# Kernel optimization log

Measured on AMD Instinct MI355X. Metric: run time of the kernel, lower is better.

## Reference

```python
import jax, jax.numpy as jnp
import numpy as np

N, E, G = 100000, 1600000, 64   # nodes, edges, graphs
IN, H, OUT = 32, 128, 3


def setup_inputs() -> dict:
    key = jax.random.key(0)
    ks = jax.random.split(key, 24)
    def w(k, i, o):
        return (jax.random.normal(k, (i, o), jnp.float32) / np.sqrt(i)).astype(jnp.float32)
    inp = {
        "x": jax.random.normal(ks[0], (N, IN), jnp.float32),
        "edge_index": jax.random.randint(ks[1], (2, E), 0, N, dtype=jnp.int32).astype(jnp.int64),
        "batch": jnp.sort(jax.random.randint(ks[2], (N,), 0, G, dtype=jnp.int32)).astype(jnp.int64),
        # SAGEConv layer 0 (in->hidden): lin_l (neighbors, with bias), lin_r (root, no bias)
        "Wl0": w(ks[3], IN, H), "bl0": jnp.zeros((H,), jnp.float32), "Wr0": w(ks[4], IN, H),
        # SAGEConv layers 1,2 (hidden->hidden)
        "Wl1": w(ks[5], H, H), "bl1": jnp.zeros((H,), jnp.float32), "Wr1": w(ks[6], H, H),
        "Wl2": w(ks[7], H, H), "bl2": jnp.zeros((H,), jnp.float32), "Wr2": w(ks[8], H, H),
        # output head
        "Wfc": w(ks[9], H, OUT), "bfc": jnp.zeros((OUT,), jnp.float32),
        # aux MLP on (dim1, dim3)
        "Wa1": w(ks[10], 2, H), "ba1": jnp.zeros((H,), jnp.float32),
        "Wa2": w(ks[11], H, H), "ba2": jnp.zeros((H,), jnp.float32),
        "Wao": w(ks[12], H, 1), "bao": jnp.zeros((1,), jnp.float32),
    }
    return inp


def _sage_conv(x, src, dst, Wl, bl, Wr):
    # PyG SAGEConv (mean aggr): out = lin_l(mean_{j in N(i)} x_j) + lin_r(x_i)
    msg = x[src]                                   # [E, d] gather
    agg = jax.ops.segment_sum(msg, dst, num_segments=N)
    cnt = jax.ops.segment_sum(jnp.ones((src.shape[0],), x.dtype), dst, num_segments=N)
    mean = agg / jnp.maximum(cnt, 1.0)[:, None]
    return mean @ Wl + bl + x @ Wr


def reference(x, edge_index, batch,
              Wl0, bl0, Wr0, Wl1, bl1, Wr1, Wl2, bl2, Wr2,
              Wfc, bfc, Wa1, ba1, Wa2, ba2, Wao, bao):
    src, dst = edge_index[0], edge_index[1]
    h = jax.nn.relu(_sage_conv(x, src, dst, Wl0, bl0, Wr0))   # dropout is identity in eval
    h = jax.nn.relu(_sage_conv(h, src, dst, Wl1, bl1, Wr1))
    h = jax.nn.relu(_sage_conv(h, src, dst, Wl2, bl2, Wr2))
    main = h @ Wfc + bfc                                      # [N, 3]
    dim1, dim3 = main[:, 0], main[:, 2]
    aux_in = jnp.stack([dim1, dim3], axis=-1)                 # [N, 2]
    a = jax.nn.relu(aux_in @ Wa1 + ba1)
    a = jax.nn.relu(a @ Wa2 + ba2)
    aux_out = (a @ Wao + bao)[:, 0]                           # [N]
    final = jnp.stack([dim1, aux_out, dim3], axis=-1)         # [N, 3]
    # global mean pool over graph ids
    s = jax.ops.segment_sum(final, batch, num_segments=G)
    c = jax.ops.segment_sum(jnp.ones((final.shape[0],), final.dtype), batch, num_segments=G)
    return s / jnp.maximum(c, 1.0)[:, None]                   # [G, 3]
```

## Files before the change

kernel.cpp:

```cpp
#include <hip/hip_runtime.h>

#define NR 128
#define PART_CH 4096
typedef unsigned short ushortT;
typedef __attribute__((ext_vector_type(8))) short short8;
typedef __attribute__((ext_vector_type(4))) float float4v;
typedef __attribute__((ext_vector_type(2))) float float2v;

__device__ __forceinline__ unsigned short f32_to_bf16_rne(float f) {
    unsigned u = __float_as_uint(f);
    unsigned r = (u + 0x7fffu + ((u >> 16) & 1u)) >> 16;
    return (unsigned short)r;
}

__device__ __forceinline__ unsigned char f32_to_fp8(float f) {
    return (unsigned char)(__builtin_amdgcn_cvt_pk_fp8_f32(f, f, 0, false) & 0xff);
}

__device__ __forceinline__ void accum8(float* acc, uint4 v) {
    unsigned u[4] = {v.x, v.y, v.z, v.w};
#pragma unroll
    for (int q = 0; q < 4; q++) {
        acc[2 * q]     += __uint_as_float(u[q] << 16);
        acc[2 * q + 1] += __uint_as_float(u[q] & 0xffff0000u);
    }
}

__device__ __forceinline__ void accum16_fp8(float* acc, uint4 v) {
    unsigned u[4] = {v.x, v.y, v.z, v.w};
#pragma unroll
    for (int q = 0; q < 4; q++) {
        float2v lo = __builtin_amdgcn_cvt_pk_f32_fp8(u[q], false);
        float2v hi = __builtin_amdgcn_cvt_pk_f32_fp8(u[q], true);
        acc[4 * q + 0] += lo.x;
        acc[4 * q + 1] += lo.y;
        acc[4 * q + 2] += hi.x;
        acc[4 * q + 3] += hi.y;
    }
}


__launch_bounds__(256)
__global__ void bucket_count(const int* __restrict__ dst, int* __restrict__ bcnt, int E, int NB) {
    __shared__ int h[1024];
    int t = threadIdx.x;
    for (int j = t; j < NB; j += 256) h[j] = 0;
    __syncthreads();
    int e0 = blockIdx.x * PART_CH;
    int e1 = min(e0 + PART_CH, E);
    for (int e = e0 + t; e < e1; e += 256) atomicAdd(&h[dst[e] >> 7], 1);
    __syncthreads();
    for (int j = t; j < NB; j += 256) {
        int v = h[j];
        if (v) atomicAdd(&bcnt[j], v);
    }
}

__launch_bounds__(256)
__global__ void bucket_scan(const int* __restrict__ bcnt, int* __restrict__ bstart,
                            int* __restrict__ gcur, int NB, int E) {
    __shared__ int sh[256];
    int t = threadIdx.x;
    int v[4];
    int tot = 0;
#pragma unroll
    for (int j = 0; j < 4; j++) {
        int idx = t * 4 + j;
        v[j] = (idx < NB) ? bcnt[idx] : 0;
        tot += v[j];
    }
    sh[t] = tot;
    __syncthreads();
    for (int off = 1; off < 256; off <<= 1) {
        int add = (t >= off) ? sh[t - off] : 0;
        __syncthreads();
        sh[t] += add;
        __syncthreads();
    }
    int run = sh[t] - tot;
#pragma unroll
    for (int j = 0; j < 4; j++) {
        int idx = t * 4 + j;
        if (idx < NB) { bstart[idx] = run; gcur[idx] = run; }
        run += v[j];
    }
    if (t == 0) bstart[NB] = E;
}

__launch_bounds__(256)
__global__ void partition_edges(const int* __restrict__ src, const int* __restrict__ dst,
                                int* __restrict__ gcur, unsigned* __restrict__ packed,
                                int E, int NB) {
    __shared__ int hist[1024];
    __shared__ int base[1024];
    int t = threadIdx.x;
    int e0 = blockIdx.x * PART_CH;
    int e1 = min(e0 + PART_CH, E);
    for (int j = t; j < NB; j += 256) hist[j] = 0;
    __syncthreads();
    for (int e = e0 + t; e < e1; e += 256) atomicAdd(&hist[dst[e] >> 7], 1);
    __syncthreads();
    for (int j = t; j < NB; j += 256) {
        int h = hist[j];
        base[j] = h ? atomicAdd(&gcur[j], h) : 0;
    }
    __syncthreads();
    for (int j = t; j < NB; j += 256) hist[j] = base[j];
    __syncthreads();
    for (int e = e0 + t; e < e1; e += 256) {
        int d = dst[e];
        int b = d >> 7;
        int pos = atomicAdd(&hist[b], 1);
        packed[pos] = (unsigned)src[e] | ((unsigned)(d & (NR - 1)) << 17);
    }
}

__launch_bounds__(256)
__global__ void bucket_sort(const unsigned* __restrict__ packed, const int* __restrict__ bstart,
                            int* __restrict__ row_start, int* __restrict__ srcs, int N) {
    __shared__ int cnt[NR];
    __shared__ int sc[NR];
    __shared__ int cur[NR];
    int b = blockIdx.x, t = threadIdx.x;
    int nb0 = b * NR;
    int nnode = min(NR, N - nb0);
    int lo = bstart[b], hi = bstart[b + 1];
    if (t < NR) cnt[t] = 0;
    __syncthreads();
    for (int j = lo + t; j < hi; j += 256) atomicAdd(&cnt[packed[j] >> 17], 1);
    __syncthreads();
    if (t < NR) sc[t] = cnt[t];
    __syncthreads();
    for (int off = 1; off < NR; off <<= 1) {
        int add = (t >= off && t < NR) ? sc[t - off] : 0;
        __syncthreads();
        if (t < NR) sc[t] += add;
        __syncthreads();
    }
    if (t < nnode) {
        int s = lo + sc[t] - cnt[t];
        row_start[nb0 + t] = s;
        cur[t] = s;
    }
    if (t == 0 && nb0 + nnode == N) row_start[N] = hi;
    __syncthreads();
    for (int j = lo + t; j < hi; j += 256) {
        unsigned pk = packed[j];
        int pos = atomicAdd(&cur[pk >> 17], 1);
        srcs[pos] = (int)(pk & 0x1FFFFu);
    }
}


__global__ void to_bf16_vec(const float* __restrict__ in, ushortT* __restrict__ out, int n4) {
    int t = blockIdx.x * 256 + threadIdx.x;
    if (t < n4) {
        float4 v = ((const float4*)in)[t];
        ushort4 o;
        o.x = f32_to_bf16_rne(v.x);
        o.y = f32_to_bf16_rne(v.y);
        o.z = f32_to_bf16_rne(v.z);
        o.w = f32_to_bf16_rne(v.w);
        ((ushort4*)out)[t] = o;
    }
}


__global__ void prep_wt(const float* __restrict__ Wl, const float* __restrict__ Wr,
                        ushortT* __restrict__ Wt, int KH) {
    int KT = 2 * KH;
    int tid = blockIdx.x * 256 + threadIdx.x;
    if (tid >= 128 * KT) return;
    int col = tid / KT, k = tid - col * KT;
    float v = (k < KH) ? Wl[k * 128 + col] : Wr[(k - KH) * 128 + col];
    int pos = (k + 8 * col) & (KT - 1);
    Wt[col * KT + pos] = f32_to_bf16_rne(v);
}

__global__ void prep_w1(const float* __restrict__ W, ushortT* __restrict__ Wt) {
    int tid = blockIdx.x * 256 + threadIdx.x;
    if (tid >= 128 * 128) return;
    int col = tid >> 7, k = tid & 127;
    int pos = (k + 8 * col) & 127;
    Wt[col * 128 + pos] = f32_to_bf16_rne(W[k * 128 + col]);
}


template <int CPN>
__launch_bounds__(256)
__global__ void aggregate_mean_bf16(const uint4* __restrict__ hin, ushortT* __restrict__ out,
                                    const int* __restrict__ srcs, const int* __restrict__ rs, int n) {
    constexpr int TPN = CPN / 2;
    int tid = blockIdx.x * 256 + threadIdx.x;
    if (tid >= n * TPN) return;
    int i = tid / TPN;
    int c = tid & (TPN - 1);
    int lo = rs[i], hi = rs[i + 1];
    float acc0[8], acc1[8];
#pragma unroll
    for (int q = 0; q < 8; q++) { acc0[q] = 0.f; acc1[q] = 0.f; }
    int e = lo;
    for (; e + 8 <= hi; e += 8) {
        int s[8];
#pragma unroll
        for (int u = 0; u < 8; u++) s[u] = srcs[e + u];
        uint4 va[8], vb[8];
#pragma unroll
        for (int u = 0; u < 8; u++) {
            va[u] = hin[(size_t)s[u] * CPN + c];
            vb[u] = hin[(size_t)s[u] * CPN + c + TPN];
        }
#pragma unroll
        for (int u = 0; u < 8; u++) { accum8(acc0, va[u]); accum8(acc1, vb[u]); }
    }
    for (; e + 4 <= hi; e += 4) {
        int s[4];
#pragma unroll
        for (int u = 0; u < 4; u++) s[u] = srcs[e + u];
        uint4 va[4], vb[4];
#pragma unroll
        for (int u = 0; u < 4; u++) {
            va[u] = hin[(size_t)s[u] * CPN + c];
            vb[u] = hin[(size_t)s[u] * CPN + c + TPN];
        }
#pragma unroll
        for (int u = 0; u < 4; u++) { accum8(acc0, va[u]); accum8(acc1, vb[u]); }
    }
    for (; e < hi; ++e) {
        int s = srcs[e];
        accum8(acc0, hin[(size_t)s * CPN + c]);
        accum8(acc1, hin[(size_t)s * CPN + c + TPN]);
    }
    float inv = 1.0f / (float)max(hi - lo, 1);
    uint4 o0, o1;
    o0.x = (unsigned)f32_to_bf16_rne(acc0[0] * inv) | ((unsigned)f32_to_bf16_rne(acc0[1] * inv) << 16);
    o0.y = (unsigned)f32_to_bf16_rne(acc0[2] * inv) | ((unsigned)f32_to_bf16_rne(acc0[3] * inv) << 16);
    o0.z = (unsigned)f32_to_bf16_rne(acc0[4] * inv) | ((unsigned)f32_to_bf16_rne(acc0[5] * inv) << 16);
    o0.w = (unsigned)f32_to_bf16_rne(acc0[6] * inv) | ((unsigned)f32_to_bf16_rne(acc0[7] * inv) << 16);
    o1.x = (unsigned)f32_to_bf16_rne(acc1[0] * inv) | ((unsigned)f32_to_bf16_rne(acc1[1] * inv) << 16);
    o1.y = (unsigned)f32_to_bf16_rne(acc1[2] * inv) | ((unsigned)f32_to_bf16_rne(acc1[3] * inv) << 16);
    o1.z = (unsigned)f32_to_bf16_rne(acc1[4] * inv) | ((unsigned)f32_to_bf16_rne(acc1[5] * inv) << 16);
    o1.w = (unsigned)f32_to_bf16_rne(acc1[6] * inv) | ((unsigned)f32_to_bf16_rne(acc1[7] * inv) << 16);
    ((uint4*)out)[(size_t)i * CPN + c] = o0;
    ((uint4*)out)[(size_t)i * CPN + c + TPN] = o1;
}


__launch_bounds__(256)
__global__ void aggregate_mean_fp8(const uint4* __restrict__ hin, ushortT* __restrict__ out,
                                   const int* __restrict__ srcs, const int* __restrict__ rs, int n) {
    int tid = blockIdx.x * 256 + threadIdx.x;
    if (tid >= n * 8) return;
    int i = tid >> 3;
    int c = tid & 7;
    int lo = rs[i], hi = rs[i + 1];
    float acc[16];
#pragma unroll
    for (int q = 0; q < 16; q++) acc[q] = 0.f;
    int e = lo;
    for (; e + 8 <= hi; e += 8) {
        int s[8];
#pragma unroll
        for (int u = 0; u < 8; u++) s[u] = srcs[e + u];
        uint4 v[8];
#pragma unroll
        for (int u = 0; u < 8; u++) v[u] = hin[(size_t)s[u] * 8 + c];
#pragma unroll
        for (int u = 0; u < 8; u++) accum16_fp8(acc, v[u]);
    }
    for (; e + 4 <= hi; e += 4) {
        int s[4];
#pragma unroll
        for (int u = 0; u < 4; u++) s[u] = srcs[e + u];
        uint4 v[4];
#pragma unroll
        for (int u = 0; u < 4; u++) v[u] = hin[(size_t)s[u] * 8 + c];
#pragma unroll
        for (int u = 0; u < 4; u++) accum16_fp8(acc, v[u]);
    }
    for (; e < hi; ++e) accum16_fp8(acc, hin[(size_t)srcs[e] * 8 + c]);
    float inv = 1.0f / (float)max(hi - lo, 1);
    uint4 o0, o1;
    o0.x = (unsigned)f32_to_bf16_rne(acc[0] * inv)  | ((unsigned)f32_to_bf16_rne(acc[1] * inv) << 16);
    o0.y = (unsigned)f32_to_bf16_rne(acc[2] * inv)  | ((unsigned)f32_to_bf16_rne(acc[3] * inv) << 16);
    o0.z = (unsigned)f32_to_bf16_rne(acc[4] * inv)  | ((unsigned)f32_to_bf16_rne(acc[5] * inv) << 16);
    o0.w = (unsigned)f32_to_bf16_rne(acc[6] * inv)  | ((unsigned)f32_to_bf16_rne(acc[7] * inv) << 16);
    o1.x = (unsigned)f32_to_bf16_rne(acc[8] * inv)  | ((unsigned)f32_to_bf16_rne(acc[9] * inv) << 16);
    o1.y = (unsigned)f32_to_bf16_rne(acc[10] * inv) | ((unsigned)f32_to_bf16_rne(acc[11] * inv) << 16);
    o1.z = (unsigned)f32_to_bf16_rne(acc[12] * inv) | ((unsigned)f32_to_bf16_rne(acc[13] * inv) << 16);
    o1.w = (unsigned)f32_to_bf16_rne(acc[14] * inv) | ((unsigned)f32_to_bf16_rne(acc[15] * inv) << 16);
    ((uint4*)out)[(size_t)i * 16 + c * 2]     = o0;
    ((uint4*)out)[(size_t)i * 16 + c * 2 + 1] = o1;
}


template <int KH, bool OUT_BF16, bool OUT_FP8>
__launch_bounds__(256, 2)
__global__ void gemm_mfma(const ushortT* __restrict__ Am, const ushortT* __restrict__ Ah,
                          const ushortT* __restrict__ Wt, const float* __restrict__ bias,
                          float* __restrict__ outf, ushortT* __restrict__ outbf,
                          unsigned char* __restrict__ outf8, int n) {
    constexpr int KT = 2 * KH;
    __shared__ ushortT sW[128 * KT];
    int t = threadIdx.x;
    constexpr int TOT16 = 128 * KT * 2 / 16;
    {
        const uint4* Wg = (const uint4*)Wt;
        uint4* Ws = (uint4*)sW;
        for (int j = t; j < TOT16; j += 256) Ws[j] = Wg[j];
    }
    __syncthreads();
    int wv = t >> 6, lane = t & 63;
    int q = lane >> 4, cid = lane & 15;
    int rbase = blockIdx.x * 128 + wv * 32;
    int r0 = rbase + cid, r1 = r0 + 16;
    int r0c = min(r0, n - 1), r1c = min(r1, n - 1);
    float4v acc[2][8];
#pragma unroll
    for (int i = 0; i < 2; i++)
#pragma unroll
        for (int j = 0; j < 8; j++) acc[i][j] = (float4v){0.f, 0.f, 0.f, 0.f};
    int swz = q * 8 + 8 * cid;
#pragma unroll
    for (int ks = 0; ks < KT / 32; ++ks) {
        int kk = ks * 32;
        const ushortT* abase = (kk < KH) ? Am : Ah;
        int kc = (kk < KH) ? kk : kk - KH;
        short8 a0 = *(const short8*)(abase + (size_t)r0c * KH + kc + q * 8);
        short8 a1 = *(const short8*)(abase + (size_t)r1c * KH + kc + q * 8);
#pragma unroll
        for (int j = 0; j < 8; ++j) {
            int col = j * 16 + cid;
            int p = (kk + swz + j * 128) & (KT - 1);
            short8 b = *(const short8*)(sW + col * KT + p);
            acc[0][j] = __builtin_amdgcn_mfma_f32_16x16x32_bf16(a0, b, acc[0][j], 0, 0, 0);
            acc[1][j] = __builtin_amdgcn_mfma_f32_16x16x32_bf16(a1, b, acc[1][j], 0, 0, 0);
        }
    }
    float bo[8];
#pragma unroll
    for (int j = 0; j < 8; ++j) bo[j] = bias[j * 16 + cid];
#pragma unroll
    for (int i = 0; i < 2; ++i) {
#pragma unroll
        for (int rr = 0; rr < 4; ++rr) {
            int row = rbase + i * 16 + q * 4 + rr;
            if (row < n) {
#pragma unroll
                for (int j = 0; j < 8; ++j) {
                    int col = j * 16 + cid;
                    float v = fmaxf(acc[i][j][rr] + bo[j], 0.f);
                    if (OUT_BF16) outbf[(size_t)row * 128 + col] = f32_to_bf16_rne(v);
                    if (OUT_FP8)  outf8[(size_t)row * 128 + col] = f32_to_fp8(v);
                    if (!OUT_BF16 && !OUT_FP8) outf[(size_t)row * 128 + col] = v;
                }
            }
        }
    }
}


template <int KH>
__launch_bounds__(256, 2)
__global__ void gemm_mfma_fin(const ushortT* __restrict__ Am, const ushortT* __restrict__ Ah,
                              const ushortT* __restrict__ Wt, const float* __restrict__ bias,
                              const float* __restrict__ Wfc, const float* __restrict__ bfc,
                              float* __restrict__ fin, int n) {
    constexpr int KT = 2 * KH;
    __shared__ ushortT sW[128 * KT];
    int t = threadIdx.x;
    constexpr int TOT16 = 128 * KT * 2 / 16;
    {
        const uint4* Wg = (const uint4*)Wt;
        uint4* Ws = (uint4*)sW;
        for (int j = t; j < TOT16; j += 256) Ws[j] = Wg[j];
    }
    __syncthreads();
    int wv = t >> 6, lane = t & 63;
    int q = lane >> 4, cid = lane & 15;
    int rbase = blockIdx.x * 128 + wv * 32;
    int r0 = rbase + cid, r1 = r0 + 16;
    int r0c = min(r0, n - 1), r1c = min(r1, n - 1);
    float4v acc[2][8];
#pragma unroll
    for (int i = 0; i < 2; i++)
#pragma unroll
        for (int j = 0; j < 8; j++) acc[i][j] = (float4v){0.f, 0.f, 0.f, 0.f};
    int swz = q * 8 + 8 * cid;
#pragma unroll
    for (int ks = 0; ks < KT / 32; ++ks) {
        int kk = ks * 32;
        const ushortT* abase = (kk < KH) ? Am : Ah;
        int kc = (kk < KH) ? kk : kk - KH;
        short8 a0 = *(const short8*)(abase + (size_t)r0c * KH + kc + q * 8);
        short8 a1 = *(const short8*)(abase + (size_t)r1c * KH + kc + q * 8);
#pragma unroll
        for (int j = 0; j < 8; ++j) {
            int col = j * 16 + cid;
            int p = (kk + swz + j * 128) & (KT - 1);
            short8 b = *(const short8*)(sW + col * KT + p);
            acc[0][j] = __builtin_amdgcn_mfma_f32_16x16x32_bf16(a0, b, acc[0][j], 0, 0, 0);
            acc[1][j] = __builtin_amdgcn_mfma_f32_16x16x32_bf16(a1, b, acc[1][j], 0, 0, 0);
        }
    }
    float bo[8], w1[8], w3[8];
#pragma unroll
    for (int j = 0; j < 8; ++j) {
        int col = j * 16 + cid;
        bo[j] = bias[col];
        w1[j] = Wfc[col * 3 + 0];
        w3[j] = Wfc[col * 3 + 2];
    }
    float bfc0 = bfc[0], bfc2 = bfc[2];
#pragma unroll
    for (int i = 0; i < 2; ++i) {
#pragma unroll
        for (int rr = 0; rr < 4; ++rr) {
            float p1 = 0.f, p3 = 0.f;
#pragma unroll
            for (int j = 0; j < 8; ++j) {
                float v = fmaxf(acc[i][j][rr] + bo[j], 0.f);
                p1 += v * w1[j];
                p3 += v * w3[j];
            }
            p1 += __shfl_xor(p1, 1, 64); p3 += __shfl_xor(p3, 1, 64);
            p1 += __shfl_xor(p1, 2, 64); p3 += __shfl_xor(p3, 2, 64);
            p1 += __shfl_xor(p1, 4, 64); p3 += __shfl_xor(p3, 4, 64);
            p1 += __shfl_xor(p1, 8, 64); p3 += __shfl_xor(p3, 8, 64);
            int row = rbase + i * 16 + q * 4 + rr;
            if (cid == 0 && row < n) {
                fin[(size_t)row * 3 + 0] = p1 + bfc0;
                fin[(size_t)row * 3 + 2] = p3 + bfc2;
            }
        }
    }
}


__launch_bounds__(256, 4)
__global__ void head_mfma(const ushortT* __restrict__ Wa2t, const float* __restrict__ Wa1,
                          const float* __restrict__ ba1, const float* __restrict__ ba2,
                          const float* __restrict__ Wao, const float* __restrict__ bao,
                          float* __restrict__ fin, int n) {
    __shared__ ushortT sW[128 * 128];
    __shared__ float sD1[128], sD3[128];
    __shared__ float sWa1a[128], sWa1b[128], sBa1[128];
    int t = threadIdx.x;
    {
        const uint4* Wg = (const uint4*)Wa2t;
        uint4* Ws = (uint4*)sW;
        for (int j = t; j < 2048; j += 256) Ws[j] = Wg[j];
    }
    int rbase = blockIdx.x * 128;
    if (t < 128) {
        sWa1a[t] = Wa1[t];
        sWa1b[t] = Wa1[128 + t];
        sBa1[t] = ba1[t];
        int row = min(rbase + t, n - 1);
        sD1[t] = fin[(size_t)row * 3 + 0];
        sD3[t] = fin[(size_t)row * 3 + 2];
    }
    __syncthreads();
    int wv = t >> 6, lane = t & 63;
    int q = lane >> 4, cid = lane & 15;
    int rl0 = wv * 32 + cid, rl1 = rl0 + 16;
    float d1a = sD1[rl0], d3a = sD3[rl0];
    float d1b = sD1[rl1], d3b = sD3[rl1];
    float4v acc[2][8];
#pragma unroll
    for (int i = 0; i < 2; i++)
#pragma unroll
        for (int j = 0; j < 8; j++) acc[i][j] = (float4v){0.f, 0.f, 0.f, 0.f};
    int swz = q * 8 + 8 * cid;
#pragma unroll
    for (int ks = 0; ks < 4; ++ks) {
        int k0 = ks * 32 + q * 8;
        short8 a0, a1;
#pragma unroll
        for (int j = 0; j < 8; ++j) {
            int k = k0 + j;
            float w0 = sWa1a[k], w1 = sWa1b[k], bb = sBa1[k];
            float v0 = fmaxf(fmaf(d1a, w0, fmaf(d3a, w1, bb)), 0.f);
            float v1 = fmaxf(fmaf(d1b, w0, fmaf(d3b, w1, bb)), 0.f);
            a0[j] = (short)f32_to_bf16_rne(v0);
            a1[j] = (short)f32_to_bf16_rne(v1);
        }
        int p = (ks * 32 + swz) & 127;
#pragma unroll
        for (int j = 0; j < 8; ++j) {
            short8 b = *(const short8*)(sW + (j * 16 + cid) * 128 + p);
            acc[0][j] = __builtin_amdgcn_mfma_f32_16x16x32_bf16(a0, b, acc[0][j], 0, 0, 0);
            acc[1][j] = __builtin_amdgcn_mfma_f32_16x16x32_bf16(a1, b, acc[1][j], 0, 0, 0);
        }
    }
    float b2[8], wo[8];
#pragma unroll
    for (int j = 0; j < 8; ++j) {
        int col = j * 16 + cid;
        b2[j] = ba2[col];
        wo[j] = Wao[col];
    }
    float bao0 = bao[0];
#pragma unroll
    for (int i = 0; i < 2; ++i) {
#pragma unroll
        for (int rr = 0; rr < 4; ++rr) {
            float s = 0.f;
#pragma unroll
            for (int j = 0; j < 8; ++j) s += fmaxf(acc[i][j][rr] + b2[j], 0.f) * wo[j];
            s += __shfl_xor(s, 1, 64);
            s += __shfl_xor(s, 2, 64);
            s += __shfl_xor(s, 4, 64);
            s += __shfl_xor(s, 8, 64);
            int row = rbase + wv * 32 + i * 16 + q * 4 + rr;
            if (cid == 0 && row < n) fin[(size_t)row * 3 + 1] = s + bao0;
        }
    }
}


__global__ void pool_kernel(const float* __restrict__ fin, const int* __restrict__ batch,
                            float* __restrict__ out, int n) {
    int g = blockIdx.x, t = threadIdx.x;
    int lo = 0, hi = n;
    while (lo < hi) { int mid = (lo + hi) >> 1; if (batch[mid] < g) lo = mid + 1; else hi = mid; }
    int start = lo;
    lo = 0; hi = n;
    while (lo < hi) { int mid = (lo + hi) >> 1; if (batch[mid] < g + 1) lo = mid + 1; else hi = mid; }
    int end = lo;
    float s0 = 0.f, s1 = 0.f, s2 = 0.f;
    for (int i = start + t; i < end; i += 256) {
        s0 += fin[(size_t)i * 3 + 0];
        s1 += fin[(size_t)i * 3 + 1];
        s2 += fin[(size_t)i * 3 + 2];
    }
    __shared__ float r0[256], r1[256], r2[256];
    r0[t] = s0; r1[t] = s1; r2[t] = s2;
    __syncthreads();
    for (int off = 128; off > 0; off >>= 1) {
        if (t < off) { r0[t] += r0[t + off]; r1[t] += r1[t + off]; r2[t] += r2[t + off]; }
        __syncthreads();
    }
    if (t == 0) {
        float c = (float)max(end - start, 1);
        out[g * 3 + 0] = r0[0] / c;
        out[g * 3 + 1] = r1[0] / c;
        out[g * 3 + 2] = r2[0] / c;
    }
}


extern "C" void kernel_launch(void* const* d_in, const int* in_sizes, int n_in,
                              void* d_out, int out_size, void* d_ws, size_t ws_size,
                              hipStream_t stream) {
    const float* x    = (const float*)d_in[0];
    const int*   ei   = (const int*)d_in[1];
    const int*   batch= (const int*)d_in[2];
    const float* Wl0  = (const float*)d_in[3];
    const float* bl0  = (const float*)d_in[4];
    const float* Wr0  = (const float*)d_in[5];
    const float* Wl1  = (const float*)d_in[6];
    const float* bl1  = (const float*)d_in[7];
    const float* Wr1  = (const float*)d_in[8];
    const float* Wl2  = (const float*)d_in[9];
    const float* bl2  = (const float*)d_in[10];
    const float* Wr2  = (const float*)d_in[11];
    const float* Wfc  = (const float*)d_in[12];
    const float* bfc  = (const float*)d_in[13];
    const float* Wa1  = (const float*)d_in[14];
    const float* ba1  = (const float*)d_in[15];
    const float* Wa2  = (const float*)d_in[16];
    const float* ba2  = (const float*)d_in[17];
    const float* Wao  = (const float*)d_in[18];
    const float* bao  = (const float*)d_in[19];

    const int N = in_sizes[0] / 32;
    const int E = in_sizes[1] / 2;
    const int G = out_size / 3;
    const int* src = ei;
    const int* dst = ei + E;
    float* out = (float*)d_out;
    const int NB = (N + NR - 1) / NR;

    char* p = (char*)d_ws;
    auto carve = [&](size_t bytes) {
        void* r = (void*)p;
        p += (bytes + 255) & ~(size_t)255;
        return r;
    };
    int*           bcnt     = (int*)carve((size_t)NB * 4);
    int*           bstart   = (int*)carve((size_t)(NB + 1) * 4);
    int*           gcur     = (int*)carve((size_t)NB * 4);
    int*           row_start= (int*)carve((size_t)(N + 1) * 4);
    unsigned*      packed   = (unsigned*)carve((size_t)E * 4);
    int*           srcs     = (int*)carve((size_t)E * 4);
    ushortT*       aggbf    = (ushortT*)carve((size_t)N * 128 * 2);
    ushortT*       xbf      = (ushortT*)carve((size_t)N * 32 * 2);
    ushortT*       hbf0     = (ushortT*)carve((size_t)N * 128 * 2);
    ushortT*       hbf1     = (ushortT*)carve((size_t)N * 128 * 2);
    unsigned char* hf8_0    = (unsigned char*)carve((size_t)N * 128);
    unsigned char* hf8_1    = (unsigned char*)carve((size_t)N * 128);
    float*         fin      = (float*)carve((size_t)N * 3 * 4);
    ushortT*       Wt0      = (ushortT*)carve((size_t)128 * 64 * 2);
    ushortT*       Wt1      = (ushortT*)carve((size_t)128 * 256 * 2);
    ushortT*       Wt2      = (ushortT*)carve((size_t)128 * 256 * 2);
    ushortT*       Wa2t     = (ushortT*)carve((size_t)128 * 128 * 2);

    const int gemm_grid = (N + 127) / 128;
    const int part_grid = (E + PART_CH - 1) / PART_CH;

    to_bf16_vec<<<(N * 32 / 4 + 255) / 256, 256, 0, stream>>>(x, xbf, N * 32 / 4);
    prep_wt<<<(128 * 64 + 255) / 256, 256, 0, stream>>>(Wl0, Wr0, Wt0, 32);
    prep_wt<<<(128 * 256 + 255) / 256, 256, 0, stream>>>(Wl1, Wr1, Wt1, 128);
    prep_wt<<<(128 * 256 + 255) / 256, 256, 0, stream>>>(Wl2, Wr2, Wt2, 128);
    prep_w1<<<(128 * 128 + 255) / 256, 256, 0, stream>>>(Wa2, Wa2t);

    hipMemsetAsync(bcnt, 0, (size_t)NB * 4, stream);
    bucket_count<<<part_grid, 256, 0, stream>>>(dst, bcnt, E, NB);
    bucket_scan<<<1, 256, 0, stream>>>(bcnt, bstart, gcur, NB, E);
    partition_edges<<<part_grid, 256, 0, stream>>>(src, dst, gcur, packed, E, NB);
    bucket_sort<<<NB, 256, 0, stream>>>(packed, bstart, row_start, srcs, N);

    aggregate_mean_bf16<4><<<(N * 2 + 255) / 256, 256, 0, stream>>>(
        (const uint4*)xbf, aggbf, srcs, row_start, N);
    gemm_mfma<32, true, true><<<gemm_grid, 256, 0, stream>>>(
        aggbf, xbf, Wt0, bl0, (float*)nullptr, hbf0, hf8_0, N);
    aggregate_mean_fp8<<<(N * 8 + 255) / 256, 256, 0, stream>>>(
        (const uint4*)hf8_0, aggbf, srcs, row_start, N);
    gemm_mfma<128, true, true><<<gemm_grid, 256, 0, stream>>>(
        aggbf, hbf0, Wt1, bl1, (float*)nullptr, hbf1, hf8_1, N);
    aggregate_mean_fp8<<<(N * 8 + 255) / 256, 256, 0, stream>>>(
        (const uint4*)hf8_1, aggbf, srcs, row_start, N);
    gemm_mfma_fin<128><<<gemm_grid, 256, 0, stream>>>(
        aggbf, hbf1, Wt2, bl2, Wfc, bfc, fin, N);

    head_mfma<<<gemm_grid, 256, 0, stream>>>(
        Wa2t, Wa1, ba1, ba2, Wao, bao, fin, N);

    pool_kernel<<<G, 256, 0, stream>>>(fin, batch, out, N);
}
```

Measured before the change: 359.8 us.

## Rework edge bucketing with per-block histograms, batch loads, fuse weight prep, widen fp8 aggregation

Replaces the global atomic bucket count and scan with per-block histograms plus a single-block prefix scan. The partition step then needs no global atomics and no second histogram pass. The edge chunk size doubles, and the histogram, partition and sort loops batch 8 loads per thread before doing their shared-memory atomics, to expose more memory-level parallelism. The four weight-prep launches are merged into one kernel. The fp8 aggregation now has each thread handle 32 channels, using 4 threads per node instead of 8, and the 4-wide remainder loops are dropped. In exchange the single-thread scan walks NBLK rows serially, and the larger per-thread register footprint may lower occupancy in the gather kernels.

```diff
diff --git a/kernel.cpp b/kernel.cpp
--- a/kernel.cpp
+++ b/kernel.cpp
@@ -1,7 +1,7 @@
 #include <hip/hip_runtime.h>
 
 #define NR 128
-#define PART_CH 4096
+#define PART_CH 8192
 typedef unsigned short ushortT;
 typedef __attribute__((ext_vector_type(8))) short short8;
 typedef __attribute__((ext_vector_type(4))) float float4v;
@@ -41,77 +41,83 @@
 
 
 __launch_bounds__(256)
-__global__ void bucket_count(const int* __restrict__ dst, int* __restrict__ bcnt, int E, int NB) {
+__global__ void hist_pass(const int* __restrict__ dst, int* __restrict__ hist_blk, int E, int NB) {
     __shared__ int h[1024];
     int t = threadIdx.x;
-    for (int j = t; j < NB; j += 256) h[j] = 0;
+    for (int j = t; j < 1024; j += 256) h[j] = 0;
     __syncthreads();
     int e0 = blockIdx.x * PART_CH;
     int e1 = min(e0 + PART_CH, E);
-    for (int e = e0 + t; e < e1; e += 256) atomicAdd(&h[dst[e] >> 7], 1);
-    __syncthreads();
-    for (int j = t; j < NB; j += 256) {
-        int v = h[j];
-        if (v) atomicAdd(&bcnt[j], v);
-    }
-}
-
-__launch_bounds__(256)
-__global__ void bucket_scan(const int* __restrict__ bcnt, int* __restrict__ bstart,
-                            int* __restrict__ gcur, int NB, int E) {
-    __shared__ int sh[256];
+    for (int base = e0; base < e1; base += 2048) {
+        int idx = base + t;
+        int d[8];
+        int cnt = 0;
+#pragma unroll
+        for (int u = 0; u < 8; u++) {
+            int e = idx + u * 256;
+            if (e < e1) d[cnt++] = dst[e];
+        }
+        for (int u = 0; u < cnt; u++) atomicAdd(&h[d[u] >> 7], 1);
+    }
+    __syncthreads();
+    int* row = hist_blk + (size_t)blockIdx.x * NB;
+    for (int j = t; j < NB; j += 256) row[j] = h[j];
+}
+
+__launch_bounds__(1024)
+__global__ void pbase_scan(const int* __restrict__ hist_blk, int* __restrict__ bstart,
+                           int* __restrict__ pbase, int NB, int NBLK, int E) {
+    __shared__ int sh[1024];
     int t = threadIdx.x;
-    int v[4];
     int tot = 0;
-#pragma unroll
-    for (int j = 0; j < 4; j++) {
-        int idx = t * 4 + j;
-        v[j] = (idx < NB) ? bcnt[idx] : 0;
-        tot += v[j];
-    }
+    if (t < NB)
+        for (int b = 0; b < NBLK; b++) tot += hist_blk[(size_t)b * NB + t];
     sh[t] = tot;
     __syncthreads();
-    for (int off = 1; off < 256; off <<= 1) {
+    for (int off = 1; off < 1024; off <<= 1) {
         int add = (t >= off) ? sh[t - off] : 0;
         __syncthreads();
         sh[t] += add;
         __syncthreads();
     }
-    int run = sh[t] - tot;
-#pragma unroll
-    for (int j = 0; j < 4; j++) {
-        int idx = t * 4 + j;
-        if (idx < NB) { bstart[idx] = run; gcur[idx] = run; }
-        run += v[j];
+    int excl = sh[t] - tot;
+    if (t < NB) {
+        bstart[t] = excl;
+        int run = excl;
+        for (int b = 0; b < NBLK; b++) {
+            size_t idx = (size_t)b * NB + t;
+            pbase[idx] = run;
+            run += hist_blk[idx];
+        }
     }
     if (t == 0) bstart[NB] = E;
 }
 
 __launch_bounds__(256)
 __global__ void partition_edges(const int* __restrict__ src, const int* __restrict__ dst,
-                                int* __restrict__ gcur, unsigned* __restrict__ packed,
+                                const int* __restrict__ pbase, unsigned* __restrict__ packed,
                                 int E, int NB) {
-    __shared__ int hist[1024];
-    __shared__ int base[1024];
-    int t = threadIdx.x;
-    int e0 = blockIdx.x * PART_CH;
+    __shared__ int cur[1024];
+    int t = threadIdx.x, b = blockIdx.x;
+    const int* prow = pbase + (size_t)b * NB;
+    for (int j = t; j < NB; j += 256) cur[j] = prow[j];
+    __syncthreads();
+    int e0 = b * PART_CH;
     int e1 = min(e0 + PART_CH, E);
-    for (int j = t; j < NB; j += 256) hist[j] = 0;
-    __syncthreads();
-    for (int e = e0 + t; e < e1; e += 256) atomicAdd(&hist[dst[e] >> 7], 1);
-    __syncthreads();
-    for (int j = t; j < NB; j += 256) {
-        int h = hist[j];
-        base[j] = h ? atomicAdd(&gcur[j], h) : 0;
-    }
-    __syncthreads();
-    for (int j = t; j < NB; j += 256) hist[j] = base[j];
-    __syncthreads();
-    for (int e = e0 + t; e < e1; e += 256) {
-        int d = dst[e];
-        int b = d >> 7;
-        int pos = atomicAdd(&hist[b], 1);
-        packed[pos] = (unsigned)src[e] | ((unsigned)(d & (NR - 1)) << 17);
+    for (int base = e0; base < e1; base += 2048) {
+        int idx = base + t;
+        int d[8], s[8];
+        int cnt = 0;
+#pragma unroll
+        for (int u = 0; u < 8; u++) {
+            int e = idx + u * 256;
+            if (e < e1) { d[cnt] = dst[e]; s[cnt] = src[e]; cnt++; }
+        }
+        for (int u = 0; u < cnt; u++) {
+            int dd = d[u];
+            int pos = atomicAdd(&cur[dd >> 7], 1);
+            packed[pos] = (unsigned)s[u] | ((unsigned)(dd & (NR - 1)) << 17);
+        }
     }
 }
 
@@ -127,7 +133,17 @@
     int lo = bstart[b], hi = bstart[b + 1];
     if (t < NR) cnt[t] = 0;
     __syncthreads();
-    for (int j = lo + t; j < hi; j += 256) atomicAdd(&cnt[packed[j] >> 17], 1);
+    for (int base = lo; base < hi; base += 2048) {
+        int idx = base + t;
+        unsigned pk[8];
+        int c = 0;
+#pragma unroll
+        for (int u = 0; u < 8; u++) {
+            int e = idx + u * 256;
+            if (e < hi) pk[c++] = packed[e];
+        }
+        for (int u = 0; u < c; u++) atomicAdd(&cnt[pk[u] >> 17], 1);
+    }
     __syncthreads();
     if (t < NR) sc[t] = cnt[t];
     __syncthreads();
@@ -144,10 +160,19 @@
     }
     if (t == 0 && nb0 + nnode == N) row_start[N] = hi;
     __syncthreads();
-    for (int j = lo + t; j < hi; j += 256) {
-        unsigned pk = packed[j];
-        int pos = atomicAdd(&cur[pk >> 17], 1);
-        srcs[pos] = (int)(pk & 0x1FFFFu);
+    for (int base = lo; base < hi; base += 2048) {
+        int idx = base + t;
+        unsigned pk[8];
+        int c = 0;
+#pragma unroll
+        for (int u = 0; u < 8; u++) {
+            int e = idx + u * 256;
+            if (e < hi) pk[c++] = packed[e];
+        }
+        for (int u = 0; u < c; u++) {
+            int pos = atomicAdd(&cur[pk[u] >> 17], 1);
+            srcs[pos] = (int)(pk[u] & 0x1FFFFu);
+        }
     }
 }
 
@@ -166,23 +191,32 @@
 }
 
 
-__global__ void prep_wt(const float* __restrict__ Wl, const float* __restrict__ Wr,
-                        ushortT* __restrict__ Wt, int KH) {
-    int KT = 2 * KH;
+__global__ void prep_all(const float* __restrict__ Wl0, const float* __restrict__ Wr0,
+                         const float* __restrict__ Wl1, const float* __restrict__ Wr1,
+                         const float* __restrict__ Wl2, const float* __restrict__ Wr2,
+                         const float* __restrict__ Wa2,
+                         ushortT* __restrict__ Wt0, ushortT* __restrict__ Wt1,
+                         ushortT* __restrict__ Wt2, ushortT* __restrict__ Wa2t) {
     int tid = blockIdx.x * 256 + threadIdx.x;
-    if (tid >= 128 * KT) return;
-    int col = tid / KT, k = tid - col * KT;
-    float v = (k < KH) ? Wl[k * 128 + col] : Wr[(k - KH) * 128 + col];
-    int pos = (k + 8 * col) & (KT - 1);
-    Wt[col * KT + pos] = f32_to_bf16_rne(v);
-}
-
-__global__ void prep_w1(const float* __restrict__ W, ushortT* __restrict__ Wt) {
-    int tid = blockIdx.x * 256 + threadIdx.x;
-    if (tid >= 128 * 128) return;
-    int col = tid >> 7, k = tid & 127;
-    int pos = (k + 8 * col) & 127;
-    Wt[col * 128 + pos] = f32_to_bf16_rne(W[k * 128 + col]);
+    if (tid < 8192) {
+        int col = tid >> 6, k = tid & 63;
+        float v = (k < 32) ? Wl0[k * 128 + col] : Wr0[(k - 32) * 128 + col];
+        Wt0[col * 64 + ((k + 8 * col) & 63)] = f32_to_bf16_rne(v);
+    } else if (tid < 8192 + 32768) {
+        int j = tid - 8192;
+        int col = j >> 8, k = j & 255;
+        float v = (k < 128) ? Wl1[k * 128 + col] : Wr1[(k - 128) * 128 + col];
+        Wt1[col * 256 + ((k + 8 * col) & 255)] = f32_to_bf16_rne(v);
+    } else if (tid < 8192 + 65536) {
+        int j = tid - 8192 - 32768;
+        int col = j >> 8, k = j & 255;
+        float v = (k < 128) ? Wl2[k * 128 + col] : Wr2[(k - 128) * 128 + col];
+        Wt2[col * 256 + ((k + 8 * col) & 255)] = f32_to_bf16_rne(v);
+    } else if (tid < 8192 + 65536 + 16384) {
+        int j = tid - 8192 - 65536;
+        int col = j >> 7, k = j & 127;
+        Wa2t[col * 128 + ((k + 8 * col) & 127)] = f32_to_bf16_rne(Wa2[k * 128 + col]);
+    }
 }
 
 
@@ -212,19 +246,6 @@
         }
 #pragma unroll
         for (int u = 0; u < 8; u++) { accum8(acc0, va[u]); accum8(acc1, vb[u]); }
-    }
-    for (; e + 4 <= hi; e += 4) {
-        int s[4];
-#pragma unroll
-        for (int u = 0; u < 4; u++) s[u] = srcs[e + u];
-        uint4 va[4], vb[4];
-#pragma unroll
-        for (int u = 0; u < 4; u++) {
-            va[u] = hin[(size_t)s[u] * CPN + c];
-            vb[u] = hin[(size_t)s[u] * CPN + c + TPN];
-        }
-#pragma unroll
-        for (int u = 0; u < 4; u++) { accum8(acc0, va[u]); accum8(acc1, vb[u]); }
     }
     for (; e < hi; ++e) {
         int s = srcs[e];
@@ -250,47 +271,49 @@
 __global__ void aggregate_mean_fp8(const uint4* __restrict__ hin, ushortT* __restrict__ out,
                                    const int* __restrict__ srcs, const int* __restrict__ rs, int n) {
     int tid = blockIdx.x * 256 + threadIdx.x;
-    if (tid >= n * 8) return;
-    int i = tid >> 3;
-    int c = tid & 7;
+    if (tid >= n * 4) return;
+    int i = tid >> 2;
+    int c = tid & 3;
     int lo = rs[i], hi = rs[i + 1];
-    float acc[16];
-#pragma unroll
-    for (int q = 0; q < 16; q++) acc[q] = 0.f;
+    float acc0[16], acc1[16];
+#pragma unroll
+    for (int q = 0; q < 16; q++) { acc0[q] = 0.f; acc1[q] = 0.f; }
     int e = lo;
     for (; e + 8 <= hi; e += 8) {
         int s[8];
 #pragma unroll
         for (int u = 0; u < 8; u++) s[u] = srcs[e + u];
-        uint4 v[8];
-#pragma unroll
-        for (int u = 0; u < 8; u++) v[u] = hin[(size_t)s[u] * 8 + c];
-#pragma unroll
-        for (int u = 0; u < 8; u++) accum16_fp8(acc, v[u]);
-    }
-    for (; e + 4 <= hi; e += 4) {
-        int s[4];
-#pragma unroll
-        for (int u = 0; u < 4; u++) s[u] = srcs[e + u];
-        uint4 v[4];
-#pragma unroll
-        for (int u = 0; u < 4; u++) v[u] = hin[(size_t)s[u] * 8 + c];
-#pragma unroll
-        for (int u = 0; u < 4; u++) accum16_fp8(acc, v[u]);
-    }
-    for (; e < hi; ++e) accum16_fp8(acc, hin[(size_t)srcs[e] * 8 + c]);
+        uint4 va[8], vb[8];
+#pragma unroll
+        for (int u = 0; u < 8; u++) {
+            va[u] = hin[(size_t)s[u] * 8 + c];
+            vb[u] = hin[(size_t)s[u] * 8 + c + 4];
+        }
+#pragma unroll
+        for (int u = 0; u < 8; u++) { accum16_fp8(acc0, va[u]); accum16_fp8(acc1, vb[u]); }
+    }
+    for (; e < hi; ++e) {
+        int s = srcs[e];
+        accum16_fp8(acc0, hin[(size_t)s * 8 + c]);
+        accum16_fp8(acc1, hin[(size_t)s * 8 + c + 4]);
+    }
     float inv = 1.0f / (float)max(hi - lo, 1);
-    uint4 o0, o1;
-    o0.x = (unsigned)f32_to_bf16_rne(acc[0] * inv)  | ((unsigned)f32_to_bf16_rne(acc[1] * inv) << 16);
-    o0.y = (unsigned)f32_to_bf16_rne(acc[2] * inv)  | ((unsigned)f32_to_bf16_rne(acc[3] * inv) << 16);
-    o0.z = (unsigned)f32_to_bf16_rne(acc[4] * inv)  | ((unsigned)f32_to_bf16_rne(acc[5] * inv) << 16);
-    o0.w = (unsigned)f32_to_bf16_rne(acc[6] * inv)  | ((unsigned)f32_to_bf16_rne(acc[7] * inv) << 16);
-    o1.x = (unsigned)f32_to_bf16_rne(acc[8] * inv)  | ((unsigned)f32_to_bf16_rne(acc[9] * inv) << 16);
-    o1.y = (unsigned)f32_to_bf16_rne(acc[10] * inv) | ((unsigned)f32_to_bf16_rne(acc[11] * inv) << 16);
-    o1.z = (unsigned)f32_to_bf16_rne(acc[12] * inv) | ((unsigned)f32_to_bf16_rne(acc[13] * inv) << 16);
-    o1.w = (unsigned)f32_to_bf16_rne(acc[14] * inv) | ((unsigned)f32_to_bf16_rne(acc[15] * inv) << 16);
-    ((uint4*)out)[(size_t)i * 16 + c * 2]     = o0;
-    ((uint4*)out)[(size_t)i * 16 + c * 2 + 1] = o1;
+    uint4 o;
+#pragma unroll
+    for (int half = 0; half < 2; ++half) {
+        float* a = half ? acc1 : acc0;
+        int cb = half ? (2 * c + 8) : (2 * c);
+        o.x = (unsigned)f32_to_bf16_rne(a[0] * inv)  | ((unsigned)f32_to_bf16_rne(a[1] * inv) << 16);
+        o.y = (unsigned)f32_to_bf16_rne(a[2] * inv)  | ((unsigned)f32_to_bf16_rne(a[3] * inv) << 16);
+        o.z = (unsigned)f32_to_bf16_rne(a[4] * inv)  | ((unsigned)f32_to_bf16_rne(a[5] * inv) << 16);
+        o.w = (unsigned)f32_to_bf16_rne(a[6] * inv)  | ((unsigned)f32_to_bf16_rne(a[7] * inv) << 16);
+        ((uint4*)out)[(size_t)i * 16 + cb] = o;
+        o.x = (unsigned)f32_to_bf16_rne(a[8] * inv)  | ((unsigned)f32_to_bf16_rne(a[9] * inv) << 16);
+        o.y = (unsigned)f32_to_bf16_rne(a[10] * inv) | ((unsigned)f32_to_bf16_rne(a[11] * inv) << 16);
+        o.z = (unsigned)f32_to_bf16_rne(a[12] * inv) | ((unsigned)f32_to_bf16_rne(a[13] * inv) << 16);
+        o.w = (unsigned)f32_to_bf16_rne(a[14] * inv) | ((unsigned)f32_to_bf16_rne(a[15] * inv) << 16);
+        ((uint4*)out)[(size_t)i * 16 + cb + 1] = o;
+    }
 }
 
 
@@ -581,6 +604,7 @@
     const int* dst = ei + E;
     float* out = (float*)d_out;
     const int NB = (N + NR - 1) / NR;
+    const int NBLK = (E + PART_CH - 1) / PART_CH;
 
     char* p = (char*)d_ws;
     auto carve = [&](size_t bytes) {
@@ -588,9 +612,9 @@
         p += (bytes + 255) & ~(size_t)255;
         return r;
     };
-    int*           bcnt     = (int*)carve((size_t)NB * 4);
+    int*           hist_blk = (int*)carve((size_t)NBLK * NB * 4);
+    int*           pbase    = (int*)carve((size_t)NBLK * NB * 4);
     int*           bstart   = (int*)carve((size_t)(NB + 1) * 4);
-    int*           gcur     = (int*)carve((size_t)NB * 4);
     int*           row_start= (int*)carve((size_t)(N + 1) * 4);
     unsigned*      packed   = (unsigned*)carve((size_t)E * 4);
     int*           srcs     = (int*)carve((size_t)E * 4);
@@ -607,29 +631,25 @@
     ushortT*       Wa2t     = (ushortT*)carve((size_t)128 * 128 * 2);
 
     const int gemm_grid = (N + 127) / 128;
-    const int part_grid = (E + PART_CH - 1) / PART_CH;
 
     to_bf16_vec<<<(N * 32 / 4 + 255) / 256, 256, 0, stream>>>(x, xbf, N * 32 / 4);
-    prep_wt<<<(128 * 64 + 255) / 256, 256, 0, stream>>>(Wl0, Wr0, Wt0, 32);
-    prep_wt<<<(128 * 256 + 255) / 256, 256, 0, stream>>>(Wl1, Wr1, Wt1, 128);
-    prep_wt<<<(128 * 256 + 255) / 256, 256, 0, stream>>>(Wl2, Wr2, Wt2, 128);
-    prep_w1<<<(128 * 128 + 255) / 256, 256, 0, stream>>>(Wa2, Wa2t);
-
-    hipMemsetAsync(bcnt, 0, (size_t)NB * 4, stream);
-    bucket_count<<<part_grid, 256, 0, stream>>>(dst, bcnt, E, NB);
-    bucket_scan<<<1, 256, 0, stream>>>(bcnt, bstart, gcur, NB, E);
-    partition_edges<<<part_grid, 256, 0, stream>>>(src, dst, gcur, packed, E, NB);
+    prep_all<<<(8192 + 65536 + 16384 + 255) / 256, 256, 0, stream>>>(
+        Wl0, Wr0, Wl1, Wr1, Wl2, Wr2, Wa2, Wt0, Wt1, Wt2, Wa2t);
+
+    hist_pass<<<NBLK, 256, 0, stream>>>(dst, hist_blk, E, NB);
+    pbase_scan<<<1, 1024, 0, stream>>>(hist_blk, bstart, pbase, NB, NBLK, E);
+    partition_edges<<<NBLK, 256, 0, stream>>>(src, dst, pbase, packed, E, NB);
     bucket_sort<<<NB, 256, 0, stream>>>(packed, bstart, row_start, srcs, N);
 
     aggregate_mean_bf16<4><<<(N * 2 + 255) / 256, 256, 0, stream>>>(
         (const uint4*)xbf, aggbf, srcs, row_start, N);
     gemm_mfma<32, true, true><<<gemm_grid, 256, 0, stream>>>(
         aggbf, xbf, Wt0, bl0, (float*)nullptr, hbf0, hf8_0, N);
-    aggregate_mean_fp8<<<(N * 8 + 255) / 256, 256, 0, stream>>>(
+    aggregate_mean_fp8<<<(N * 4 + 255) / 256, 256, 0, stream>>>(
         (const uint4*)hf8_0, aggbf, srcs, row_start, N);
     gemm_mfma<128, true, true><<<gemm_grid, 256, 0, stream>>>(
         aggbf, hbf0, Wt1, bl1, (float*)nullptr, hbf1, hf8_1, N);
-    aggregate_mean_fp8<<<(N * 8 + 255) / 256, 256, 0, stream>>>(
+    aggregate_mean_fp8<<<(N * 4 + 255) / 256, 256, 0, stream>>>(
         (const uint4*)hf8_1, aggbf, srcs, row_start, N);
     gemm_mfma_fin<128><<<gemm_grid, 256, 0, stream>>>(
         aggbf, hbf1, Wt2, bl2, Wfc, bfc, fin, N);
```

Measured after the change: 488.1 us. +35.7%, slower.
